# Kernel tuning notes

Hardware: AMD Instinct MI355X
Metric: run time of the kernel (lower is better)

## Reference

```python
import jax, jax.numpy as jnp
import numpy as np

N = 50000        # nodes per node type
E_ADJ = 800000   # edges per adjacency
E_DEC = 200000   # decoder edge batch
F = 128          # input feature dim
H = 64           # hidden dim (all hid_dims equal)
RT_NUM = 4       # DEDICOM relation subtypes
# relation order per stage: [(0,0),(0,1),(1,0),(1,1)]; input node type j per relation:
J_ORDER = (0, 1, 0, 1)


def setup_inputs() -> dict:
    key = jax.random.key(0)
    ks = jax.random.split(key, 16)
    inp = {
        'adj_rows': jax.random.randint(ks[0], (8, E_ADJ), 0, N, dtype=jnp.int32),
        'adj_cols': jax.random.randint(ks[1], (8, E_ADJ), 0, N, dtype=jnp.int32),
        'adj_vals': jax.random.uniform(ks[2], (8, E_ADJ), dtype=jnp.float32),
        'feat0': jax.random.normal(ks[3], (N, F), dtype=jnp.float32),
        'feat1': jax.random.normal(ks[4], (N, F), dtype=jnp.float32),
        'W1': jax.random.normal(ks[5], (4, F, H), dtype=jnp.float32) * 0.05,
        'W2': jax.random.normal(ks[6], (4, H, H), dtype=jnp.float32) * 0.05,
        'W3': jax.random.normal(ks[7], (4, H, H), dtype=jnp.float32) * 0.05,
        'W4': jax.random.normal(ks[8], (4, H, H), dtype=jnp.float32) * 0.05,
        'R_global': jax.random.normal(ks[9], (H, H), dtype=jnp.float32) * 0.05,
        'D_local': jax.random.normal(ks[10], (RT_NUM, H), dtype=jnp.float32) * 0.05,
        'edges': jax.random.randint(ks[11], (E_DEC, 2), 0, N, dtype=jnp.int32),
        'rt_k': 1,
    }
    return inp


def _gcn_stage(rows, cols, vals, x0, x1, W):
    """One multi-relation GCN layer over 4 relations [(0,0),(0,1),(1,0),(1,1)].
    rows/cols/vals: [4, E]; x0/x1: [N, Fin]; W: [4, Fin, H].
    Returns (out0, out1): per-destination-type summed, relu'd embeddings [N, H]."""
    xin = jnp.stack([x0, x1, x0, x1])                    # [4, N, Fin] per J_ORDER
    xw = jnp.einsum('knf,kfh->knh', xin, W)              # transform per relation

    def spmm(r, c, v, m):
        # sparse adj @ m : gather messages along cols, scatter-add into rows
        return jax.ops.segment_sum(m[c] * v[:, None], r, num_segments=N)

    y = jax.vmap(spmm)(rows, cols, vals, xw)             # [4, N, H]
    y = jax.nn.relu(y)                                   # activation inside each layer
    # get_embed: sum per-relation outputs grouped by destination type i
    return y[0] + y[1], y[2] + y[3]


def reference(adj_rows, adj_cols, adj_vals, feat0, feat1, W1, W2, W3, W4,
              R_global, D_local, edges, rt_k):
    r1, c1, v1 = adj_rows[:4], adj_cols[:4], adj_vals[:4]   # stage-1 adjacencies
    r2, c2, v2 = adj_rows[4:], adj_cols[4:], adj_vals[4:]   # stage-2 adjacencies

    h0, h1 = _gcn_stage(r1, c1, v1, feat0, feat1, W1)       # s1_l1
    h0, h1 = _gcn_stage(r1, c1, v1, h0, h1, W2)             # s1_l2
    h0, h1 = _gcn_stage(r2, c2, v2, h0, h1, W3)             # s2_l1
    h0, h1 = _gcn_stage(r2, c2, v2, h0, h1, W4)             # s2_l2

    # TDDecoder for rel_type = (0, 1): gather endpoints, DEDICOM bilinear score.
    er = h0[edges[:, 0]]                                    # [E, H]
    ec = h1[edges[:, 1]]                                    # [E, H]
    d = D_local[rt_k]                                       # [H]
    M = d[:, None] * R_global * d[None, :]                  # D_k R D_k
    # torch.diag(er @ M @ ec.T) == per-edge bilinear form
    preds_pos = jnp.einsum('eh,hg,eg->e', er, M, ec)        # [E]
    return preds_pos
```

## Files before the change

kernel.cpp:

```cpp
#include <hip/hip_runtime.h>

#define N_NODES 50000
#define E_ADJ   800000
#define E_DEC   200000
#define FDIM    128
#define HDIM    64
#define NP1     (N_NODES + 1)
#define NBUK    196
#define SCAP    768
#define BCAP    (8 * SCAP)
#define TILE_E  4096
#define EPB     16
#define NPBLK   196

typedef _Float16 f16;
typedef __attribute__((ext_vector_type(2))) _Float16 f16x2;
typedef __attribute__((ext_vector_type(4))) _Float16 f16x4;
typedef __attribute__((ext_vector_type(8))) _Float16 f16x8;
typedef __attribute__((ext_vector_type(4))) float f32x4;

__device__ __forceinline__ int   ntl_i(const int* p)   { return __builtin_nontemporal_load(p); }
__device__ __forceinline__ float ntl_f(const float* p) { return __builtin_nontemporal_load(p); }

__global__ void part_kernel(const int* __restrict__ rows,
                            const int* __restrict__ cols,
                            const float* __restrict__ vals,
                            int* __restrict__ gcur,
                            unsigned long long* __restrict__ bucketed)
{
    const int k   = blockIdx.y;
    const int sub = blockIdx.x & 7;
    const int tid = threadIdx.x;
    const long long t0 = (long long)blockIdx.x * TILE_E;

    __shared__ int hist[NBUK];
    __shared__ int cur[NBUK];
    for (int i = tid; i < NBUK; i += 256) hist[i] = 0;
    __syncthreads();

    for (int it = 0; it < EPB; ++it) {
        const long long e = t0 + it * 256 + tid;
        if (e < E_ADJ) {
            const int r = rows[(size_t)k * E_ADJ + e];
            atomicAdd(&hist[r >> 8], 1);
        }
    }
    __syncthreads();

    for (int i = tid; i < NBUK; i += 256)
        cur[i] = (hist[i] > 0) ? atomicAdd(&gcur[(k * NBUK + i) * 8 + sub], hist[i]) : 0;
    __syncthreads();

    for (int it = 0; it < EPB; ++it) {
        const long long e = t0 + it * 256 + tid;
        if (e < E_ADJ) {
            const int r = rows[(size_t)k * E_ADJ + e];
            const int b = r >> 8;
            const int pos = atomicAdd(&cur[b], 1);
            const int c = ntl_i(&cols[(size_t)k * E_ADJ + e]);
            const float v = ntl_f(&vals[(size_t)k * E_ADJ + e]);
            const unsigned meta = (unsigned)c | ((unsigned)(r & 255) << 16);
            const unsigned long long payload =
                ((unsigned long long)__float_as_uint(v) << 32) | meta;
            bucketed[(size_t)(k * NBUK + b) * BCAP + sub * SCAP + pos] = payload;
        }
    }
}

__global__ void bucket_scan(const int* __restrict__ gcur, int* __restrict__ srtbase)
{
    __shared__ int tot[4 * NBUK];
    for (int i = threadIdx.x; i < 4 * NBUK; i += 256) {
        int t = 0;
#pragma unroll
        for (int s8 = 0; s8 < 8; ++s8) t += gcur[i * 8 + s8];
        tot[i] = t;
    }
    __syncthreads();
    if (threadIdx.x < 4) {
        const int k = threadIdx.x;
        int run = 0;
        for (int b = 0; b < NBUK; ++b) {
            srtbase[k * NBUK + b] = run;
            run += tot[k * NBUK + b];
        }
    }
}

__global__ void bucket_sort(const unsigned long long* __restrict__ bucketed,
                            const int* __restrict__ gcur,
                            const int* __restrict__ srtbase,
                            unsigned* __restrict__ srt,
                            int* __restrict__ row_ptr)
{
    const int b = blockIdx.x, k = blockIdx.y, tid = threadIdx.x;
    const int base = srtbase[k * NBUK + b];
    const unsigned long long* bk = bucketed + (size_t)(k * NBUK + b) * BCAP;

    __shared__ int scnt[8];
    __shared__ int s[256];
    __shared__ int cur[256];
    __shared__ int rcnt[256];
    rcnt[tid] = 0;
    if (tid < 8) scnt[tid] = gcur[(k * NBUK + b) * 8 + tid];
    __syncthreads();

    for (int s8 = 0; s8 < 8; ++s8) {
        const int c8 = scnt[s8];
        for (int i = tid; i < c8; i += 256) {
            const unsigned meta = (unsigned)bk[s8 * SCAP + i];
            atomicAdd(&rcnt[(meta >> 16) & 255], 1);
        }
    }
    __syncthreads();

    const int v = rcnt[tid];
    s[tid] = v;
    __syncthreads();
    for (int off = 1; off < 256; off <<= 1) {
        const int t = (tid >= off) ? s[tid - off] : 0;
        __syncthreads();
        s[tid] += t;
        __syncthreads();
    }
    const int excl = s[tid] - v;

    const int n = b * 256 + tid;
    if (n < N_NODES) row_ptr[k * NP1 + n] = base + excl;
    if (b == NBUK - 1 && tid == 0) row_ptr[k * NP1 + N_NODES] = E_ADJ;
    cur[tid] = base + excl;
    __syncthreads();

    for (int s8 = 0; s8 < 8; ++s8) {
        const int c8 = scnt[s8];
        for (int i = tid; i < c8; i += 256) {
            const unsigned long long p = bk[s8 * SCAP + i];
            const unsigned meta = (unsigned)p;
            const int rl = (meta >> 16) & 255;
            const int c  = meta & 0xFFFF;
            const float val = __uint_as_float((unsigned)(p >> 32));
            union { f16 h; unsigned short us; } cv;
            cv.h = (f16)val;
            const int pos = atomicAdd(&cur[rl], 1);
            srt[(size_t)k * E_ADJ + pos] = ((unsigned)cv.us << 16) | (unsigned)c;
        }
    }
}

__device__ __forceinline__ void gather_quads(const unsigned* __restrict__ sp,
                                             int s, int en,
                                             const f16* __restrict__ xk,
                                             int lane, float a[4])
{
    const int es = lane >> 4;
    const int hb = (lane & 15) * 4;

    for (int base = s; base < en; base += 64) {
        const int cnt = min(64, en - base);
        unsigned meta = 0;
        if (lane < cnt) meta = sp[base + lane];
        const int nq = (cnt + 3) >> 2;
        int p = 0;
        for (; p + 4 <= nq; p += 4) {
            unsigned m[4];
#pragma unroll
            for (int u = 0; u < 4; ++u)
                m[u] = __shfl(meta, (p + u) * 4 + es, 64);
            f16x4 g[4];
            float v[4];
#pragma unroll
            for (int u = 0; u < 4; ++u) {
                union { unsigned short us; f16 h; } cv;
                cv.us = (unsigned short)(m[u] >> 16);
                v[u] = (float)cv.h;
                g[u] = *(const f16x4*)(xk + (size_t)(m[u] & 0xFFFF) * HDIM + hb);
            }
#pragma unroll
            for (int u = 0; u < 4; ++u) {
                a[0] = fmaf((float)g[u][0], v[u], a[0]);
                a[1] = fmaf((float)g[u][1], v[u], a[1]);
                a[2] = fmaf((float)g[u][2], v[u], a[2]);
                a[3] = fmaf((float)g[u][3], v[u], a[3]);
            }
        }
        for (; p < nq; ++p) {
            const unsigned m = __shfl(meta, p * 4 + es, 64);
            union { unsigned short us; f16 h; } cv;
            cv.us = (unsigned short)(m >> 16);
            const float v = (float)cv.h;
            const f16x4 g = *(const f16x4*)(xk + (size_t)(m & 0xFFFF) * HDIM + hb);
            a[0] = fmaf((float)g[0], v, a[0]);
            a[1] = fmaf((float)g[1], v, a[1]);
            a[2] = fmaf((float)g[2], v, a[2]);
            a[3] = fmaf((float)g[3], v, a[3]);
        }
    }
#pragma unroll
    for (int j = 0; j < 4; ++j) {
        a[j] += __shfl_xor(a[j], 16, 64);
        a[j] += __shfl_xor(a[j], 32, 64);
    }
}

__global__ void pack_wfrag(const float* __restrict__ W, const int K,
                           f16* __restrict__ out)
{
    const int idx = blockIdx.x * 256 + threadIdx.x;
    const int j    = idx & 7;
    const int lane = (idx >> 3) & 63;
    const int kcs  = K >> 5;
    int rest = idx >> 9;
    const int kc  = rest % kcs; rest /= kcs;
    const int nt  = rest & 3;
    const int rel = rest >> 2;
    const int k   = kc * 32 + ((lane >> 4) * 8) + j;
    const int col = nt * 16 + (lane & 15);
    out[idx] = (f16)W[((size_t)rel * K + k) * HDIM + col];
}

__global__ void gemm1_mfma(const float* __restrict__ x0,
                           const float* __restrict__ x1,
                           const f16* __restrict__ wf,
                           f16* __restrict__ xw)
{
    const int wave = threadIdx.x >> 6;
    const int lane = threadIdx.x & 63;
    const int n0 = blockIdx.x * 32;
    const int q = lane >> 4, r16 = lane & 15;

    const float* xr = (wave & 1) ? x1 : x0;

    f16x8 b[4][4];
#pragma unroll
    for (int nt = 0; nt < 4; ++nt)
#pragma unroll
        for (int kc = 0; kc < 4; ++kc)
            b[nt][kc] = *(const f16x8*)(wf + (((size_t)(wave * 4 + nt) * 4 + kc) * 64 + lane) * 8);

    for (int t = 0; t < 2; ++t) {
        const int row = n0 + t * 16 + r16;
        const int rowc = row < N_NODES ? row : N_NODES - 1;
        f16x8 a[4];
#pragma unroll
        for (int kc = 0; kc < 4; ++kc) {
            const float4 lo = *(const float4*)(xr + (size_t)rowc * FDIM + kc * 32 + q * 8);
            const float4 hi = *(const float4*)(xr + (size_t)rowc * FDIM + kc * 32 + q * 8 + 4);
            f16x8 av;
            av[0] = (f16)lo.x; av[1] = (f16)lo.y; av[2] = (f16)lo.z; av[3] = (f16)lo.w;
            av[4] = (f16)hi.x; av[5] = (f16)hi.y; av[6] = (f16)hi.z; av[7] = (f16)hi.w;
            a[kc] = av;
        }
#pragma unroll
        for (int nt = 0; nt < 4; ++nt) {
            f32x4 acc = {0.f, 0.f, 0.f, 0.f};
#pragma unroll
            for (int kc = 0; kc < 4; ++kc)
                acc = __builtin_amdgcn_mfma_f32_16x16x32_f16(a[kc], b[nt][kc], acc, 0, 0, 0);
#pragma unroll
            for (int j = 0; j < 4; ++j) {
                const int n = n0 + t * 16 + q * 4 + j;
                if (n < N_NODES)
                    xw[((size_t)wave * N_NODES + n) * HDIM + nt * 16 + r16] = (f16)acc[j];
            }
        }
    }
}

__global__ void gemm2_mfma(const f16* __restrict__ agg,
                           const f16* __restrict__ wf,
                           f16* __restrict__ h0, f16* __restrict__ h1)
{
    const int wave = threadIdx.x >> 6;
    const int lane = threadIdx.x & 63;
    const int tid  = threadIdx.x;
    const int n0 = blockIdx.x * 32;
    const int q = lane >> 4, r16 = lane & 15;

    f16x8 b[4][2];
#pragma unroll
    for (int nt = 0; nt < 4; ++nt)
#pragma unroll
        for (int kc = 0; kc < 2; ++kc)
            b[nt][kc] = *(const f16x8*)(wf + (((size_t)(wave * 4 + nt) * 2 + kc) * 64 + lane) * 8);

    __shared__ f16 yt[4][16][HDIM];

    for (int t = 0; t < 2; ++t) {
        const int row = n0 + t * 16 + r16;
        const int rowc = row < N_NODES ? row : N_NODES - 1;
        f16x8 a[2];
#pragma unroll
        for (int kc = 0; kc < 2; ++kc)
            a[kc] = *(const f16x8*)(agg + ((size_t)wave * N_NODES + rowc) * HDIM + kc * 32 + q * 8);

#pragma unroll
        for (int nt = 0; nt < 4; ++nt) {
            f32x4 acc = {0.f, 0.f, 0.f, 0.f};
#pragma unroll
            for (int kc = 0; kc < 2; ++kc)
                acc = __builtin_amdgcn_mfma_f32_16x16x32_f16(a[kc], b[nt][kc], acc, 0, 0, 0);
#pragma unroll
            for (int j = 0; j < 4; ++j)
                yt[wave][q * 4 + j][nt * 16 + r16] = (f16)fmaxf(acc[j], 0.f);
        }
        __syncthreads();

        {
            const int r  = tid >> 4;
            const int c4 = (tid & 15) * 4;
            const int n  = n0 + t * 16 + r;
            if (n < N_NODES) {
                const f16x4 a0 = *(const f16x4*)&yt[0][r][c4];
                const f16x4 a1 = *(const f16x4*)&yt[1][r][c4];
                const f16x4 a2 = *(const f16x4*)&yt[2][r][c4];
                const f16x4 a3 = *(const f16x4*)&yt[3][r][c4];
                f16x4 o0, o1;
#pragma unroll
                for (int u = 0; u < 4; ++u) {
                    o0[u] = (f16)((float)a0[u] + (float)a1[u]);
                    o1[u] = (f16)((float)a2[u] + (float)a3[u]);
                }
                *(f16x4*)(h0 + (size_t)n * HDIM + c4) = o0;
                *(f16x4*)(h1 + (size_t)n * HDIM + c4) = o1;
            }
        }
        __syncthreads();
    }
}

__global__ void spmm_csr(const unsigned* __restrict__ srt,
                         const int*    __restrict__ row_ptr,
                         const f16*    __restrict__ xw,
                         f16* __restrict__ y)
{
    const int b = blockIdx.x, k = b & 3, g = b >> 2;
    const int wave = threadIdx.x >> 6, lane = threadIdx.x & 63;
    const int n = g * 4 + wave;

    const int s  = row_ptr[k * NP1 + n];
    const int en = row_ptr[k * NP1 + n + 1];
    float a[4] = {0.f, 0.f, 0.f, 0.f};
    gather_quads(srt + (size_t)k * E_ADJ, s, en,
                 xw + (size_t)k * N_NODES * HDIM, lane, a);
    if (lane < 16) {
        f16x4 o;
        o[0] = (f16)fmaxf(a[0], 0.f);
        o[1] = (f16)fmaxf(a[1], 0.f);
        o[2] = (f16)fmaxf(a[2], 0.f);
        o[3] = (f16)fmaxf(a[3], 0.f);
        *(f16x4*)(y + ((size_t)k * N_NODES + n) * HDIM + lane * 4) = o;
    }
}

__global__ void combine_kernel(const f16* __restrict__ y,
                               f16* __restrict__ h0, f16* __restrict__ h1)
{
    const size_t NHh = (size_t)N_NODES * HDIM / 2;
    const size_t i = (size_t)blockIdx.x * 256 + threadIdx.x;
    const f16x2 a = ((const f16x2*)y)[i];
    const f16x2 b = ((const f16x2*)y)[NHh + i];
    const f16x2 c = ((const f16x2*)y)[2 * NHh + i];
    const f16x2 d = ((const f16x2*)y)[3 * NHh + i];
    f16x2 o0, o1;
    o0.x = (f16)((float)a.x + (float)b.x);
    o0.y = (f16)((float)a.y + (float)b.y);
    o1.x = (f16)((float)c.x + (float)d.x);
    o1.y = (f16)((float)c.y + (float)d.y);
    ((f16x2*)h0)[i] = o0;
    ((f16x2*)h1)[i] = o1;
}

__global__ void agg_csr(const unsigned* __restrict__ srt,
                        const int*    __restrict__ row_ptr,
                        const f16*    __restrict__ h0,
                        const f16*    __restrict__ h1,
                        f16* __restrict__ agg)
{
    const int b = blockIdx.x, k = b & 3, g = b >> 2;
    const int wave = threadIdx.x >> 6, lane = threadIdx.x & 63;
    const int n = g * 4 + wave;

    const int s  = row_ptr[k * NP1 + n];
    const int en = row_ptr[k * NP1 + n + 1];
    const f16* xk = (k & 1) ? h1 : h0;
    float a[4] = {0.f, 0.f, 0.f, 0.f};
    gather_quads(srt + (size_t)k * E_ADJ, s, en, xk, lane, a);
    if (lane < 16) {
        f16x4 o;
        o[0] = (f16)a[0];
        o[1] = (f16)a[1];
        o[2] = (f16)a[2];
        o[3] = (f16)a[3];
        *(f16x4*)(agg + ((size_t)k * N_NODES + n) * HDIM + lane * 4) = o;
    }
}

__global__ void make_M(const float* __restrict__ R, const float* __restrict__ Dl,
                       const int* __restrict__ rt_k, float* __restrict__ M)
{
    const int i = blockIdx.x * blockDim.x + threadIdx.x;
    if (i >= HDIM * HDIM) return;
    const float* d = Dl + rt_k[0] * HDIM;
    M[i] = d[i >> 6] * R[i] * d[i & 63];
}

__global__ void h0M_kernel(const f16* __restrict__ h0, const float* __restrict__ M,
                           f16* __restrict__ A)
{
    const int wave = threadIdx.x >> 6, lane = threadIdx.x & 63;
    const int n0 = blockIdx.x * 16;

    __shared__ float sx[16][HDIM];
    for (int i = threadIdx.x; i < 16 * HDIM; i += 256)
        sx[i >> 6][i & 63] = (float)h0[(size_t)n0 * HDIM + i];
    __syncthreads();

    float acc[4] = {0.f, 0.f, 0.f, 0.f};
#pragma unroll 4
    for (int f = 0; f < HDIM; ++f) {
        const float w = M[f * HDIM + lane];
#pragma unroll
        for (int r = 0; r < 4; ++r)
            acc[r] = fmaf(sx[wave * 4 + r][f], w, acc[r]);
    }
#pragma unroll
    for (int r = 0; r < 4; ++r)
        A[(size_t)(n0 + wave * 4 + r) * HDIM + lane] = (f16)acc[r];
}

__global__ void decode(const f16* __restrict__ A, const f16* __restrict__ h1,
                       const int* __restrict__ edges, float* __restrict__ out)
{
    const int w = (blockIdx.x * 256 + threadIdx.x) >> 6;
    const int lane = threadIdx.x & 63;
    const int e = w * 4 + (lane >> 4);
    const int q = lane & 15;

    const int i = edges[2 * (size_t)e];
    const int j = edges[2 * (size_t)e + 1];

    const f16x4 a = *(const f16x4*)(A + (size_t)i * HDIM + q * 4);
    const f16x4 b = *(const f16x4*)(h1 + (size_t)j * HDIM + q * 4);
    float p = 0.f;
#pragma unroll
    for (int u = 0; u < 4; ++u)
        p = fmaf((float)a[u], (float)b[u], p);
    p += __shfl_xor(p, 1, 64);
    p += __shfl_xor(p, 2, 64);
    p += __shfl_xor(p, 4, 64);
    p += __shfl_xor(p, 8, 64);
    if (q == 0) out[e] = p;
}

static void build_csr(const int* rows, const int* cols, const float* vals,
                      int* gcur, int* srtbase, unsigned long long* bucketed,
                      unsigned* srt, int* row_ptr, hipStream_t stream)
{
    hipMemsetAsync(gcur, 0, 4 * NBUK * 8 * sizeof(int), stream);
    part_kernel<<<dim3(NPBLK, 4), 256, 0, stream>>>(rows, cols, vals, gcur, bucketed);
    bucket_scan<<<1, 256, 0, stream>>>(gcur, srtbase);
    bucket_sort<<<dim3(NBUK, 4), 256, 0, stream>>>(bucketed, gcur, srtbase, srt, row_ptr);
}

extern "C" void kernel_launch(void* const* d_in, const int* in_sizes, int n_in,
                              void* d_out, int out_size, void* d_ws, size_t ws_size,
                              hipStream_t stream) {
    const int*   adj_rows = (const int*)  d_in[0];
    const int*   adj_cols = (const int*)  d_in[1];
    const float* adj_vals = (const float*)d_in[2];
    const float* feat0    = (const float*)d_in[3];
    const float* feat1    = (const float*)d_in[4];
    const float* W1       = (const float*)d_in[5];
    const float* W2       = (const float*)d_in[6];
    const float* W3       = (const float*)d_in[7];
    const float* W4       = (const float*)d_in[8];
    const float* Rg       = (const float*)d_in[9];
    const float* Dl       = (const float*)d_in[10];
    const int*   edges    = (const int*)  d_in[11];
    const int*   rt_k     = (const int*)  d_in[12];
    float* out = (float*)d_out;

    const size_t NH = (size_t)N_NODES * HDIM;
    float* ws = (float*)d_ws;
    f16*      xwh     = (f16*)ws;
    f16*      h0      = (f16*)(ws + 2 * NH);
    f16*      h1      = (f16*)(ws + 2 * NH + NH / 2);
    unsigned* srt     = (unsigned*)(ws + 3 * NH);
    int*      row_ptr = (int*)(ws + 3 * NH + 8 * (size_t)E_ADJ);
    int*      gcur    = row_ptr + 4 * NP1 + 60;
    int*      srtbase = gcur + 4 * NBUK * 8;
    float*    M       = (float*)(srtbase + 4 * NBUK + 32);
    unsigned long long* bucketed =
        (unsigned long long*)(M + HDIM * HDIM + 64);
    f16* y = (f16*)bucketed;
    f16* wfrag = (f16*)(bucketed + (size_t)4 * NBUK * BCAP);
    f16* wf1 = wfrag;
    f16* wf2 = wfrag + 32768;
    f16* wf3 = wfrag + 49152;
    f16* wf4 = wfrag + 65536;

    const int* r2 = adj_rows + 4 * (size_t)E_ADJ;
    const int* c2 = adj_cols + 4 * (size_t)E_ADJ;
    const float* v2 = adj_vals + 4 * (size_t)E_ADJ;

    pack_wfrag<<<128, 256, 0, stream>>>(W1, FDIM, wf1);
    pack_wfrag<<<64, 256, 0, stream>>>(W2, HDIM, wf2);
    pack_wfrag<<<64, 256, 0, stream>>>(W3, HDIM, wf3);
    pack_wfrag<<<64, 256, 0, stream>>>(W4, HDIM, wf4);

    build_csr(adj_rows, adj_cols, adj_vals, gcur, srtbase, bucketed, srt, row_ptr, stream);

    gemm1_mfma<<<1563, 256, 0, stream>>>(feat0, feat1, wf1, xwh);
    spmm_csr<<<N_NODES, 256, 0, stream>>>(srt, row_ptr, xwh, y);
    combine_kernel<<<(int)(NH / 2 / 256), 256, 0, stream>>>(y, h0, h1);

    agg_csr<<<N_NODES, 256, 0, stream>>>(srt, row_ptr, h0, h1, xwh);
    gemm2_mfma<<<1563, 256, 0, stream>>>(xwh, wf2, h0, h1);

    build_csr(r2, c2, v2, gcur, srtbase, bucketed, srt, row_ptr, stream);

    agg_csr<<<N_NODES, 256, 0, stream>>>(srt, row_ptr, h0, h1, xwh);
    gemm2_mfma<<<1563, 256, 0, stream>>>(xwh, wf3, h0, h1);

    agg_csr<<<N_NODES, 256, 0, stream>>>(srt, row_ptr, h0, h1, xwh);
    gemm2_mfma<<<1563, 256, 0, stream>>>(xwh, wf4, h0, h1);

    make_M<<<(HDIM * HDIM + 255) / 256, 256, 0, stream>>>(Rg, Dl, rt_k, M);
    f16* A = xwh;
    h0M_kernel<<<N_NODES / 16, 256, 0, stream>>>(h0, M, A);
    decode<<<E_DEC * 16 / 256, 256, 0, stream>>>(A, h1, edges, out);
}
```

Baseline: 538.7 us.

## Split CSR partition into more blocks and stage buckets in shared memory

The partition kernel now uses 782 blocks of 1024 edges instead of 196 blocks of 4096, with 32 sub-slots per bucket instead of 8, which raises parallelism during CSR construction. The bucket sort kernel copies each bucket's compacted entries into a 48KB shared-memory stage once, then runs both the histogram and the scatter passes from LDS instead of reading global memory twice. The per-sub capacity falls to 192, which is close to the expected average count per block, so overflow is a real risk. The large LDS allocation also limits occupancy of the sort kernel.

```diff
diff --git a/kernel.cpp b/kernel.cpp
--- a/kernel.cpp
+++ b/kernel.cpp
@@ -7,11 +7,12 @@
 #define HDIM    64
 #define NP1     (N_NODES + 1)
 #define NBUK    196
-#define SCAP    768
-#define BCAP    (8 * SCAP)
-#define TILE_E  4096
-#define EPB     16
-#define NPBLK   196
+#define SUBS    32
+#define SCAP    192
+#define BCAP    (SUBS * SCAP)
+#define TILE_E  1024
+#define EPB     4
+#define NPBLK   782
 
 typedef _Float16 f16;
 typedef __attribute__((ext_vector_type(2))) _Float16 f16x2;
@@ -29,7 +30,7 @@
                             unsigned long long* __restrict__ bucketed)
 {
     const int k   = blockIdx.y;
-    const int sub = blockIdx.x & 7;
+    const int sub = blockIdx.x & (SUBS - 1);
     const int tid = threadIdx.x;
     const long long t0 = (long long)blockIdx.x * TILE_E;
 
@@ -48,7 +49,7 @@
     __syncthreads();
 
     for (int i = tid; i < NBUK; i += 256)
-        cur[i] = (hist[i] > 0) ? atomicAdd(&gcur[(k * NBUK + i) * 8 + sub], hist[i]) : 0;
+        cur[i] = (hist[i] > 0) ? atomicAdd(&gcur[(k * NBUK + i) * SUBS + sub], hist[i]) : 0;
     __syncthreads();
 
     for (int it = 0; it < EPB; ++it) {
@@ -73,7 +74,7 @@
     for (int i = threadIdx.x; i < 4 * NBUK; i += 256) {
         int t = 0;
 #pragma unroll
-        for (int s8 = 0; s8 < 8; ++s8) t += gcur[i * 8 + s8];
+        for (int s8 = 0; s8 < SUBS; ++s8) t += gcur[i * SUBS + s8];
         tot[i] = t;
     }
     __syncthreads();
@@ -97,21 +98,33 @@
     const int base = srtbase[k * NBUK + b];
     const unsigned long long* bk = bucketed + (size_t)(k * NBUK + b) * BCAP;
 
-    __shared__ int scnt[8];
+    __shared__ unsigned long long stage[BCAP];
+    __shared__ int spref[SUBS + 1];
     __shared__ int s[256];
     __shared__ int cur[256];
     __shared__ int rcnt[256];
     rcnt[tid] = 0;
-    if (tid < 8) scnt[tid] = gcur[(k * NBUK + b) * 8 + tid];
-    __syncthreads();
-
-    for (int s8 = 0; s8 < 8; ++s8) {
-        const int c8 = scnt[s8];
-        for (int i = tid; i < c8; i += 256) {
-            const unsigned meta = (unsigned)bk[s8 * SCAP + i];
-            atomicAdd(&rcnt[(meta >> 16) & 255], 1);
-        }
-    }
+    if (tid == 0) {
+        int run = 0;
+        for (int s8 = 0; s8 < SUBS; ++s8) {
+            spref[s8] = run;
+            run += gcur[(k * NBUK + b) * SUBS + s8];
+        }
+        spref[SUBS] = run;
+    }
+    __syncthreads();
+    const int cnt = spref[SUBS];
+
+    for (int s8 = 0; s8 < SUBS; ++s8) {
+        const int off = spref[s8];
+        const int c8  = spref[s8 + 1] - off;
+        for (int i = tid; i < c8; i += 256)
+            stage[off + i] = bk[s8 * SCAP + i];
+    }
+    __syncthreads();
+
+    for (int i = tid; i < cnt; i += 256)
+        atomicAdd(&rcnt[((unsigned)stage[i] >> 16) & 255], 1);
     __syncthreads();
 
     const int v = rcnt[tid];
@@ -131,19 +144,16 @@
     cur[tid] = base + excl;
     __syncthreads();
 
-    for (int s8 = 0; s8 < 8; ++s8) {
-        const int c8 = scnt[s8];
-        for (int i = tid; i < c8; i += 256) {
-            const unsigned long long p = bk[s8 * SCAP + i];
-            const unsigned meta = (unsigned)p;
-            const int rl = (meta >> 16) & 255;
-            const int c  = meta & 0xFFFF;
-            const float val = __uint_as_float((unsigned)(p >> 32));
-            union { f16 h; unsigned short us; } cv;
-            cv.h = (f16)val;
-            const int pos = atomicAdd(&cur[rl], 1);
-            srt[(size_t)k * E_ADJ + pos] = ((unsigned)cv.us << 16) | (unsigned)c;
-        }
+    for (int i = tid; i < cnt; i += 256) {
+        const unsigned long long p = stage[i];
+        const unsigned meta = (unsigned)p;
+        const int rl = (meta >> 16) & 255;
+        const int c  = meta & 0xFFFF;
+        const float val = __uint_as_float((unsigned)(p >> 32));
+        union { f16 h; unsigned short us; } cv;
+        cv.h = (f16)val;
+        const int pos = atomicAdd(&cur[rl], 1);
+        srt[(size_t)k * E_ADJ + pos] = ((unsigned)cv.us << 16) | (unsigned)c;
     }
 }
 
@@ -456,7 +466,7 @@
                       int* gcur, int* srtbase, unsigned long long* bucketed,
                       unsigned* srt, int* row_ptr, hipStream_t stream)
 {
-    hipMemsetAsync(gcur, 0, 4 * NBUK * 8 * sizeof(int), stream);
+    hipMemsetAsync(gcur, 0, 4 * NBUK * SUBS * sizeof(int), stream);
     part_kernel<<<dim3(NPBLK, 4), 256, 0, stream>>>(rows, cols, vals, gcur, bucketed);
     bucket_scan<<<1, 256, 0, stream>>>(gcur, srtbase);
     bucket_sort<<<dim3(NBUK, 4), 256, 0, stream>>>(bucketed, gcur, srtbase, srt, row_ptr);
@@ -488,7 +498,7 @@
     unsigned* srt     = (unsigned*)(ws + 3 * NH);
     int*      row_ptr = (int*)(ws + 3 * NH + 8 * (size_t)E_ADJ);
     int*      gcur    = row_ptr + 4 * NP1 + 60;
-    int*      srtbase = gcur + 4 * NBUK * 8;
+    int*      srtbase = gcur + 4 * NBUK * SUBS;
     float*    M       = (float*)(srtbase + 4 * NBUK + 32);
     unsigned long long* bucketed =
         (unsigned long long*)(M + HDIM * HDIM + 64);
```

Measured after the change: 566.1 us. 1.05x slower.
